# Kernel optimization log

Hardware: AMD Instinct MI355X
Metric: run time of the kernel (lower is better)

The kernel has to match this reference:

```python
import jax, jax.numpy as jnp
import numpy as np

D_MODEL = 2048
D_FF = 8192
N_EXPERTS = 4
B, S = 2, 2048


def setup_inputs() -> dict:
    key = jax.random.key(0)
    ks = jax.random.split(key, 6)
    scale = 0.02
    return {
        "hidden_states": jax.random.normal(ks[0], (B, S, D_MODEL), dtype=jnp.float32),
        "Wr": jax.random.normal(ks[1], (D_MODEL, N_EXPERTS), dtype=jnp.float32) * scale,
        "br": jnp.zeros((N_EXPERTS,), dtype=jnp.float32),
        "Wg": jax.random.normal(ks[2], (N_EXPERTS, D_MODEL, D_FF), dtype=jnp.float32) * scale,
        "Wu": jax.random.normal(ks[3], (N_EXPERTS, D_MODEL, D_FF), dtype=jnp.float32) * scale,
        "Wd": jax.random.normal(ks[4], (N_EXPERTS, D_FF, D_MODEL), dtype=jnp.float32) * scale,
    }


def reference(hidden_states, Wr, br, Wg, Wu, Wd):
    b, s, d = hidden_states.shape
    x = hidden_states.reshape(-1, d)  # [T, d]

    # Router: top-1 over softmax probabilities
    logits = x @ Wr + br                      # [T, E]
    probs = jax.nn.softmax(logits, axis=-1)   # [T, E]
    top_w, top_idx = jax.lax.top_k(probs, 1)  # [T, 1], [T, 1]

    # Mistral gated MLP per expert, computed densely then selected (same math
    # as masked gather -> expert MLP -> masked_scatter with top-1 routing).
    g = jnp.einsum('td,edf->tef', x, Wg)      # [T, E, f]
    u = jnp.einsum('td,edf->tef', x, Wu)      # [T, E, f]
    h = jax.nn.silu(g) * u                    # [T, E, f]
    y = jnp.einsum('tef,efd->ted', h, Wd)     # [T, E, d]

    sel = jnp.take_along_axis(y, top_idx[:, :, None], axis=1)[:, 0]  # [T, d]
    out = sel * top_w                          # scale by top-1 routing weight
    return out.reshape(b, s, d)
```

## Files before the change

kernel.cpp:

```cpp
#include <hip/hip_runtime.h>

#define T_TOK 4096
#define DM 2048
#define DF 8192
#define NE 4
#define BM 256
#define BN 64
#define BKO 32
#define BKN 64
#define MAX_TILES 20
#define PADROWS 256
#define LDK (BKO + 8)
#define NXCD 8

typedef __attribute__((ext_vector_type(8))) short short8;
typedef __attribute__((ext_vector_type(4))) float f32x4;

__device__ __forceinline__ unsigned short f2bf(float f) {
  unsigned int u = __float_as_uint(f);
  u += 0x7fffu + ((u >> 16) & 1u);
  return (unsigned short)(u >> 16);
}

__device__ __forceinline__ void gld_lds16(const unsigned short* g, unsigned short* l) {
  __builtin_amdgcn_global_load_lds(
      (const __attribute__((address_space(1))) unsigned int*)g,
      (__attribute__((address_space(3))) unsigned int*)l, 16, 0, 0);
}

__global__ __launch_bounds__(256) void router_kernel(
    const float* __restrict__ x, const float* __restrict__ Wr,
    const float* __restrict__ br, int* __restrict__ top_idx,
    float* __restrict__ top_w, int* __restrict__ counts) {
  int tok = (blockIdx.x * blockDim.x + threadIdx.x) >> 6;
  int lane = threadIdx.x & 63;
  if (tok >= T_TOK) return;
  const float* xr = x + (size_t)tok * DM;
  float s0 = 0.f, s1 = 0.f, s2 = 0.f, s3 = 0.f;
  for (int j = lane; j < DM; j += 64) {
    float xv = xr[j];
    float4 w = *(const float4*)(Wr + (size_t)j * NE);
    s0 += xv * w.x; s1 += xv * w.y; s2 += xv * w.z; s3 += xv * w.w;
  }
#pragma unroll
  for (int off = 32; off > 0; off >>= 1) {
    s0 += __shfl_xor(s0, off);
    s1 += __shfl_xor(s1, off);
    s2 += __shfl_xor(s2, off);
    s3 += __shfl_xor(s3, off);
  }
  if (lane == 0) {
    float l[NE] = {s0 + br[0], s1 + br[1], s2 + br[2], s3 + br[3]};
    int bi = 0; float bm = l[0];
#pragma unroll
    for (int e = 1; e < NE; e++) if (l[e] > bm) { bm = l[e]; bi = e; }
    float s = 0.f;
#pragma unroll
    for (int e = 0; e < NE; e++) s += __expf(l[e] - bm);
    top_idx[tok] = bi;
    top_w[tok] = 1.0f / s;
    atomicAdd(&counts[bi], 1);
  }
}

__global__ void scan_kernel(const int* __restrict__ counts, int* __restrict__ offs,
                            int* __restrict__ cursors, int* __restrict__ tiles) {
  if (threadIdx.x != 0 || blockIdx.x != 0) return;
  int offv[NE + 1];
  offv[0] = 0;
  for (int e = 0; e < NE; e++) offv[e + 1] = offv[e] + counts[e];
  for (int e = 0; e <= NE; e++) offs[e] = offv[e];
  for (int e = 0; e < NE; e++) cursors[e] = offv[e];
  int nt = 0;
  for (int e = 0; e < NE; e++) {
    int c = counts[e];
    for (int s = 0; s < c; s += BM) {
      tiles[nt * 3 + 0] = e;
      tiles[nt * 3 + 1] = offv[e] + s;
      tiles[nt * 3 + 2] = (c - s < BM) ? (c - s) : BM;
      nt++;
    }
  }
  for (; nt < MAX_TILES; nt++) {
    tiles[nt * 3 + 0] = 0; tiles[nt * 3 + 1] = 0; tiles[nt * 3 + 2] = 0;
  }
}

__global__ __launch_bounds__(256) void scatter_kernel(
    const int* __restrict__ top_idx, int* __restrict__ cursors,
    int* __restrict__ sorted) {
  int t = blockIdx.x * blockDim.x + threadIdx.x;
  if (t >= T_TOK) return;
  int e = top_idx[t];
  int p = atomicAdd(&cursors[e], 1);
  sorted[p] = t;
}

__global__ __launch_bounds__(256) void gather_x_kernel(
    const float* __restrict__ x, const int* __restrict__ sorted,
    unsigned short* __restrict__ xs) {
  const int row = blockIdx.x;
  const int t = threadIdx.x;
  unsigned short* orow = xs + (size_t)row * DM + (t << 3);
  if (row >= T_TOK) {
    short8 z = (short8){0,0,0,0,0,0,0,0};
    *(short8*)orow = z;
    return;
  }
  const float* irow = x + (size_t)sorted[row] * DM + (t << 3);
  float4 a = *(const float4*)irow;
  float4 b = *(const float4*)(irow + 4);
  short8 p;
  p[0] = (short)f2bf(a.x); p[1] = (short)f2bf(a.y);
  p[2] = (short)f2bf(a.z); p[3] = (short)f2bf(a.w);
  p[4] = (short)f2bf(b.x); p[5] = (short)f2bf(b.y);
  p[6] = (short)f2bf(b.z); p[7] = (short)f2bf(b.w);
  *(short8*)orow = p;
}

__global__ __launch_bounds__(256) void transpose_cvt_kernel(
    const float* __restrict__ in, unsigned short* __restrict__ out, int R, int C) {
  __shared__ float tile[64][68];
  const size_t eo = (size_t)blockIdx.z * (size_t)R * (size_t)C;
  const float* inp = in + eo;
  unsigned short* outp = out + eo;
  const int r0 = blockIdx.y << 6, c0 = blockIdx.x << 6;
  const int t = threadIdx.x;
  const int lrow = t >> 4, lcol = (t & 15) << 2;
#pragma unroll
  for (int i = 0; i < 4; i++) {
    float4 v = *(const float4*)(inp + (size_t)(r0 + (i << 4) + lrow) * C + c0 + lcol);
    *(float4*)&tile[(i << 4) + lrow][lcol] = v;
  }
  __syncthreads();
  const int gg = t & 7, cc = t >> 3;
#pragma unroll
  for (int cp = 0; cp < 2; cp++) {
    int c = cc + (cp << 5);
    short8 pv;
#pragma unroll
    for (int i = 0; i < 8; i++) pv[i] = (short)f2bf(tile[(gg << 3) + i][c]);
    *(short8*)(outp + (size_t)(c0 + c) * R + r0 + (gg << 3)) = pv;
  }
}

__global__ __launch_bounds__(512, 4) void gemm1_bf16_kernel(
    const unsigned short* __restrict__ xs, const unsigned short* __restrict__ wg,
    const unsigned short* __restrict__ wu, const int* __restrict__ tiles,
    unsigned short* __restrict__ hbuf) {
  const int bid = blockIdx.x;
  const int xcd = bid & (NXCD - 1);
  const int idx = bid >> 3;
  const int slot = idx % MAX_TILES;
  const int y = (xcd << 4) + idx / MAX_TILES;
  const int n0 = y * BN;

  const int e = tiles[slot * 3 + 0];
  const int row0 = tiles[slot * 3 + 1];
  const int nvalid = tiles[slot * 3 + 2];
  if (nvalid == 0) return;

  __shared__ __align__(16) unsigned short As[BM * BKN];
  __shared__ __align__(16) unsigned short Bg[BN * BKN];
  __shared__ __align__(16) unsigned short Bu[BN * BKN];

  const int t = threadIdx.x;
  const int w = t >> 6, lane = t & 63;
  const int l3 = lane >> 3, l7 = lane & 7;
  const int swz = l7 ^ l3;
  const int lr = lane & 15;
  const int wrow = (w >> 1) << 6, wcol = (w & 1) << 5;

  const unsigned short* wge = wg + (size_t)e * DM * DF;
  const unsigned short* wue = wu + (size_t)e * DM * DF;

  const unsigned short* aSrc = xs + (size_t)(row0 + (w << 5) + l3) * DM + (swz << 3);
  const unsigned short* bgSrc = wge + (size_t)(n0 + (w << 3) + l3) * DM + (swz << 3);
  const unsigned short* buSrc = wue + (size_t)(n0 + (w << 3) + l3) * DM + (swz << 3);

  f32x4 accg[4][2], accu[4][2];
#pragma unroll
  for (int mi = 0; mi < 4; mi++)
#pragma unroll
    for (int ni = 0; ni < 2; ni++) {
      accg[mi][ni] = (f32x4){0.f, 0.f, 0.f, 0.f};
      accu[mi][ni] = (f32x4){0.f, 0.f, 0.f, 0.f};
    }

  for (int k0 = 0; k0 < DM; k0 += BKN) {
#pragma unroll
    for (int j = 0; j < 4; j++)
      gld_lds16(aSrc + (size_t)(j << 3) * DM + k0, &As[(((w << 2) + j) << 9)]);
    gld_lds16(bgSrc + k0, &Bg[w << 9]);
    gld_lds16(buSrc + k0, &Bu[w << 9]);
    __syncthreads();

#pragma unroll
    for (int h = 0; h < 2; h++) {
      const int gbase = (h << 2) + (lane >> 4);
      const int g = gbase ^ (lr & 7);
      short8 af[4], bgf[2], buf2[2];
#pragma unroll
      for (int mi = 0; mi < 4; mi++) {
        int row = wrow + (mi << 4) + lr;
        af[mi] = *(const short8*)&As[(row << 6) + (g << 3)];
      }
#pragma unroll
      for (int ni = 0; ni < 2; ni++) {
        int row = wcol + (ni << 4) + lr;
        bgf[ni]  = *(const short8*)&Bg[(row << 6) + (g << 3)];
        buf2[ni] = *(const short8*)&Bu[(row << 6) + (g << 3)];
      }
#pragma unroll
      for (int mi = 0; mi < 4; mi++)
#pragma unroll
        for (int ni = 0; ni < 2; ni++) {
          accg[mi][ni] = __builtin_amdgcn_mfma_f32_16x16x32_bf16(af[mi], bgf[ni], accg[mi][ni], 0, 0, 0);
          accu[mi][ni] = __builtin_amdgcn_mfma_f32_16x16x32_bf16(af[mi], buf2[ni], accu[mi][ni], 0, 0, 0);
        }
    }
    __syncthreads();
  }

  const int l4 = (lane >> 4) << 2;
#pragma unroll
  for (int mi = 0; mi < 4; mi++) {
#pragma unroll
    for (int r = 0; r < 4; r++) {
      int lrow = wrow + (mi << 4) + l4 + r;
      if (lrow < nvalid) {
        size_t base = (size_t)(row0 + lrow) * DF + n0 + wcol + lr;
#pragma unroll
        for (int ni = 0; ni < 2; ni++) {
          float gv = accg[mi][ni][r];
          float uv = accu[mi][ni][r];
          float hv = (gv / (1.f + __expf(-gv))) * uv;
          hbuf[base + (ni << 4)] = f2bf(hv);
        }
      }
    }
  }
}

__global__ __launch_bounds__(512, 4) void gemm2_bf16_kernel(
    const unsigned short* __restrict__ hbuf, const unsigned short* __restrict__ wd,
    const int* __restrict__ tiles, const int* __restrict__ sorted,
    const float* __restrict__ topw, float* __restrict__ out) {
  const int bid = blockIdx.x;
  const int xcd = bid & (NXCD - 1);
  const int idx = bid >> 3;
  const int slot = idx % MAX_TILES;
  const int y = (xcd << 2) + idx / MAX_TILES;
  const int n0 = y * BN;

  const int e = tiles[slot * 3 + 0];
  const int row0 = tiles[slot * 3 + 1];
  const int nvalid = tiles[slot * 3 + 2];
  if (nvalid == 0) return;

  __shared__ __align__(16) unsigned short As[BM * BKN];
  __shared__ __align__(16) unsigned short Bs[BN * BKN];

  const int t = threadIdx.x;
  const int w = t >> 6, lane = t & 63;
  const int l3 = lane >> 3, l7 = lane & 7;
  const int swz = l7 ^ l3;
  const int lr = lane & 15;
  const int wrow = (w >> 1) << 6, wcol = (w & 1) << 5;

  const unsigned short* wde = wd + (size_t)e * DM * DF;
  const unsigned short* aSrc = hbuf + (size_t)(row0 + (w << 5) + l3) * DF + (swz << 3);
  const unsigned short* bSrc = wde + (size_t)(n0 + (w << 3) + l3) * DF + (swz << 3);

  f32x4 acc[4][2];
#pragma unroll
  for (int mi = 0; mi < 4; mi++)
#pragma unroll
    for (int ni = 0; ni < 2; ni++) acc[mi][ni] = (f32x4){0.f, 0.f, 0.f, 0.f};

  for (int k0 = 0; k0 < DF; k0 += BKN) {
#pragma unroll
    for (int j = 0; j < 4; j++)
      gld_lds16(aSrc + (size_t)(j << 3) * DF + k0, &As[(((w << 2) + j) << 9)]);
    gld_lds16(bSrc + k0, &Bs[w << 9]);
    __syncthreads();

#pragma unroll
    for (int h = 0; h < 2; h++) {
      const int gbase = (h << 2) + (lane >> 4);
      const int g = gbase ^ (lr & 7);
      short8 af[4], bf2[2];
#pragma unroll
      for (int mi = 0; mi < 4; mi++) {
        int row = wrow + (mi << 4) + lr;
        af[mi] = *(const short8*)&As[(row << 6) + (g << 3)];
      }
#pragma unroll
      for (int ni = 0; ni < 2; ni++) {
        int row = wcol + (ni << 4) + lr;
        bf2[ni] = *(const short8*)&Bs[(row << 6) + (g << 3)];
      }
#pragma unroll
      for (int mi = 0; mi < 4; mi++)
#pragma unroll
        for (int ni = 0; ni < 2; ni++)
          acc[mi][ni] = __builtin_amdgcn_mfma_f32_16x16x32_bf16(af[mi], bf2[ni], acc[mi][ni], 0, 0, 0);
    }
    __syncthreads();
  }

  const int l4 = (lane >> 4) << 2;
#pragma unroll
  for (int mi = 0; mi < 4; mi++) {
#pragma unroll
    for (int r = 0; r < 4; r++) {
      int lrow = wrow + (mi << 4) + l4 + r;
      if (lrow < nvalid) {
        int tok = sorted[row0 + lrow];
        float wv = topw[tok];
        size_t base = (size_t)tok * DM + n0 + wcol + lr;
#pragma unroll
        for (int ni = 0; ni < 2; ni++)
          out[base + (ni << 4)] = acc[mi][ni][r] * wv;
      }
    }
  }
}

__global__ __launch_bounds__(512, 4) void gemm1_f32_kernel(
    const float* __restrict__ x, const float* __restrict__ Wg,
    const float* __restrict__ Wu, const int* __restrict__ tiles,
    const int* __restrict__ sorted, unsigned short* __restrict__ hbuf) {
  const int slot = blockIdx.x;
  const int e = tiles[slot * 3 + 0];
  const int row0 = tiles[slot * 3 + 1];
  const int nvalid = tiles[slot * 3 + 2];
  if (nvalid == 0) return;
  const int n0 = blockIdx.y * BN;

  __shared__ __align__(16) unsigned short As[BM][LDK];
  __shared__ __align__(16) unsigned short Bg[BN][LDK];
  __shared__ __align__(16) unsigned short Bu[BN][LDK];

  const int t = threadIdx.x;
  const int arow = t >> 1;
  const int ah = (t & 1) << 4;
  const int atok = (arow < nvalid) ? sorted[row0 + arow] : -1;
  const float* __restrict__ xrow = x + (size_t)(atok >= 0 ? atok : 0) * DM;
  const int bn = t & 63;
  const int bkq = (t >> 6) << 2;

  const size_t eo = (size_t)e * DM * DF;
  const float* __restrict__ Wge = Wg + eo;
  const float* __restrict__ Wue = Wu + eo;

  const int wv = t >> 6, lane = t & 63;
  const int wrow = (wv >> 1) << 6, wcol = (wv & 1) << 5;
  const int lr = lane & 15, lk = (lane >> 4) << 3;

  f32x4 accg[4][2], accu[4][2];
#pragma unroll
  for (int mi = 0; mi < 4; mi++)
#pragma unroll
    for (int ni = 0; ni < 2; ni++) {
      accg[mi][ni] = (f32x4){0.f, 0.f, 0.f, 0.f};
      accu[mi][ni] = (f32x4){0.f, 0.f, 0.f, 0.f};
    }

  for (int k0 = 0; k0 < DM; k0 += BKO) {
#pragma unroll
    for (int j = 0; j < 4; j++) {
      float4 v = make_float4(0.f, 0.f, 0.f, 0.f);
      if (atok >= 0) v = *(const float4*)(xrow + k0 + ah + (j << 2));
      ushort4 pv;
      pv.x = f2bf(v.x); pv.y = f2bf(v.y); pv.z = f2bf(v.z); pv.w = f2bf(v.w);
      *(ushort4*)&As[arow][ah + (j << 2)] = pv;
    }
    {
      const float* pg = Wge + (size_t)(k0 + bkq) * DF + n0 + bn;
      const float* pu = Wue + (size_t)(k0 + bkq) * DF + n0 + bn;
      ushort4 vg, vu;
      vg.x = f2bf(pg[0]);              vu.x = f2bf(pu[0]);
      vg.y = f2bf(pg[(size_t)DF]);     vu.y = f2bf(pu[(size_t)DF]);
      vg.z = f2bf(pg[(size_t)2 * DF]); vu.z = f2bf(pu[(size_t)2 * DF]);
      vg.w = f2bf(pg[(size_t)3 * DF]); vu.w = f2bf(pu[(size_t)3 * DF]);
      *(ushort4*)&Bg[bn][bkq] = vg;
      *(ushort4*)&Bu[bn][bkq] = vu;
    }
    __syncthreads();

    short8 af[4], bgf[2], buf2[2];
#pragma unroll
    for (int mi = 0; mi < 4; mi++)
      af[mi] = *(const short8*)&As[wrow + (mi << 4) + lr][lk];
#pragma unroll
    for (int ni = 0; ni < 2; ni++) {
      bgf[ni]  = *(const short8*)&Bg[wcol + (ni << 4) + lr][lk];
      buf2[ni] = *(const short8*)&Bu[wcol + (ni << 4) + lr][lk];
    }
#pragma unroll
    for (int mi = 0; mi < 4; mi++)
#pragma unroll
      for (int ni = 0; ni < 2; ni++) {
        accg[mi][ni] = __builtin_amdgcn_mfma_f32_16x16x32_bf16(af[mi], bgf[ni], accg[mi][ni], 0, 0, 0);
        accu[mi][ni] = __builtin_amdgcn_mfma_f32_16x16x32_bf16(af[mi], buf2[ni], accu[mi][ni], 0, 0, 0);
      }
    __syncthreads();
  }

  const int l4 = (lane >> 4) << 2;
#pragma unroll
  for (int mi = 0; mi < 4; mi++) {
#pragma unroll
    for (int r = 0; r < 4; r++) {
      int lrow = wrow + (mi << 4) + l4 + r;
      if (lrow < nvalid) {
        size_t base = (size_t)(row0 + lrow) * DF + n0 + wcol + lr;
#pragma unroll
        for (int ni = 0; ni < 2; ni++) {
          float g = accg[mi][ni][r];
          float u = accu[mi][ni][r];
          float hv = (g / (1.f + __expf(-g))) * u;
          hbuf[base + (ni << 4)] = f2bf(hv);
        }
      }
    }
  }
}

__global__ __launch_bounds__(512, 4) void gemm2_f32_kernel(
    const unsigned short* __restrict__ hbuf, const float* __restrict__ Wd,
    const int* __restrict__ tiles, const int* __restrict__ sorted,
    const float* __restrict__ topw, float* __restrict__ out) {
  const int slot = blockIdx.x;
  const int e = tiles[slot * 3 + 0];
  const int row0 = tiles[slot * 3 + 1];
  const int nvalid = tiles[slot * 3 + 2];
  if (nvalid == 0) return;
  const int n0 = blockIdx.y * BN;

  __shared__ __align__(16) unsigned short As[BM][LDK];
  __shared__ __align__(16) unsigned short Bs[BN][LDK];

  const int t = threadIdx.x;
  const int arow = t >> 1;
  const int ah = (t & 1) << 4;
  const int bn = t & 63;
  const int bkq = (t >> 6) << 2;
  const float* __restrict__ Wde = Wd + (size_t)e * DF * DM;

  const int wv = t >> 6, lane = t & 63;
  const int wrow = (wv >> 1) << 6, wcol = (wv & 1) << 5;
  const int lr = lane & 15, lk = (lane >> 4) << 3;

  f32x4 acc[4][2];
#pragma unroll
  for (int mi = 0; mi < 4; mi++)
#pragma unroll
    for (int ni = 0; ni < 2; ni++) acc[mi][ni] = (f32x4){0.f, 0.f, 0.f, 0.f};

  const unsigned short* __restrict__ hrow =
      hbuf + (size_t)(row0 + (arow < nvalid ? arow : 0)) * DF;

  for (int k0 = 0; k0 < DF; k0 += BKO) {
    {
      short8 v0 = (short8){0,0,0,0,0,0,0,0}, v1 = v0;
      if (arow < nvalid) {
        v0 = *(const short8*)(hrow + k0 + ah);
        v1 = *(const short8*)(hrow + k0 + ah + 8);
      }
      *(short8*)&As[arow][ah] = v0;
      *(short8*)&As[arow][ah + 8] = v1;
    }
    {
      const float* pd = Wde + (size_t)(k0 + bkq) * DM + n0 + bn;
      ushort4 vd;
      vd.x = f2bf(pd[0]);
      vd.y = f2bf(pd[(size_t)DM]);
      vd.z = f2bf(pd[(size_t)2 * DM]);
      vd.w = f2bf(pd[(size_t)3 * DM]);
      *(ushort4*)&Bs[bn][bkq] = vd;
    }
    __syncthreads();

    short8 af[4], bf2[2];
#pragma unroll
    for (int mi = 0; mi < 4; mi++)
      af[mi] = *(const short8*)&As[wrow + (mi << 4) + lr][lk];
#pragma unroll
    for (int ni = 0; ni < 2; ni++)
      bf2[ni] = *(const short8*)&Bs[wcol + (ni << 4) + lr][lk];
#pragma unroll
    for (int mi = 0; mi < 4; mi++)
#pragma unroll
      for (int ni = 0; ni < 2; ni++)
        acc[mi][ni] = __builtin_amdgcn_mfma_f32_16x16x32_bf16(af[mi], bf2[ni], acc[mi][ni], 0, 0, 0);
    __syncthreads();
  }

  const int l4 = (lane >> 4) << 2;
#pragma unroll
  for (int mi = 0; mi < 4; mi++) {
#pragma unroll
    for (int r = 0; r < 4; r++) {
      int lrow = wrow + (mi << 4) + l4 + r;
      if (lrow < nvalid) {
        int tok = sorted[row0 + lrow];
        float w = topw[tok];
        size_t base = (size_t)tok * DM + n0 + wcol + lr;
#pragma unroll
        for (int ni = 0; ni < 2; ni++)
          out[base + (ni << 4)] = acc[mi][ni][r] * w;
      }
    }
  }
}

extern "C" void kernel_launch(void* const* d_in, const int* in_sizes, int n_in,
                              void* d_out, int out_size, void* d_ws, size_t ws_size,
                              hipStream_t stream) {
  const float* x  = (const float*)d_in[0];
  const float* Wr = (const float*)d_in[1];
  const float* br = (const float*)d_in[2];
  const float* Wg = (const float*)d_in[3];
  const float* Wu = (const float*)d_in[4];
  const float* Wd = (const float*)d_in[5];
  float* out = (float*)d_out;

  const size_t XS_ELEMS = (size_t)(T_TOK + PADROWS) * DM;
  const size_t HB_ELEMS = (size_t)(T_TOK + PADROWS) * DF;
  const size_t W_ELEMS  = (size_t)NE * DM * DF;
  const size_t NEED = (XS_ELEMS + HB_ELEMS + 3 * W_ELEMS) * 2 + (1 << 20);

  if (ws_size >= NEED) {
    unsigned short* xs = (unsigned short*)d_ws;
    unsigned short* hb = xs + XS_ELEMS;
    unsigned short* wg = hb + HB_ELEMS;
    unsigned short* wu = wg + W_ELEMS;
    unsigned short* wd = wu + W_ELEMS;
    int* meta = (int*)(wd + W_ELEMS);
    int* top_idx = meta;
    int* sorted  = meta + 4096;
    int* counts  = meta + 8192;
    int* offs    = meta + 8196;
    int* cursors = meta + 8201;
    int* tiles   = meta + 8208;
    float* topw  = (float*)(meta + 8320);

    hipMemsetAsync(counts, 0, NE * sizeof(int), stream);
    router_kernel<<<dim3((T_TOK * 64) / 256), 256, 0, stream>>>(x, Wr, br, top_idx, topw, counts);
    scan_kernel<<<1, 1, 0, stream>>>(counts, offs, cursors, tiles);
    scatter_kernel<<<dim3(T_TOK / 256), 256, 0, stream>>>(top_idx, cursors, sorted);
    gather_x_kernel<<<dim3(T_TOK + PADROWS), 256, 0, stream>>>(x, sorted, xs);
    transpose_cvt_kernel<<<dim3(DF / 64, DM / 64, NE), 256, 0, stream>>>(Wg, wg, DM, DF);
    transpose_cvt_kernel<<<dim3(DF / 64, DM / 64, NE), 256, 0, stream>>>(Wu, wu, DM, DF);
    transpose_cvt_kernel<<<dim3(DM / 64, DF / 64, NE), 256, 0, stream>>>(Wd, wd, DF, DM);
    gemm1_bf16_kernel<<<dim3(MAX_TILES * (DF / BN)), 512, 0, stream>>>(xs, wg, wu, tiles, hb);
    gemm2_bf16_kernel<<<dim3(MAX_TILES * (DM / BN)), 512, 0, stream>>>(hb, wd, tiles, sorted, topw, out);
  } else {
    const size_t H_BYTES = (size_t)T_TOK * DF * 2;
    unsigned short* hbuf = (unsigned short*)d_ws;
    int* meta = (int*)((char*)d_ws + H_BYTES);
    int* top_idx = meta;
    int* sorted  = meta + 4096;
    int* counts  = meta + 8192;
    int* offs    = meta + 8196;
    int* cursors = meta + 8201;
    int* tiles   = meta + 8208;
    float* topw  = (float*)(meta + 8320);

    hipMemsetAsync(counts, 0, NE * sizeof(int), stream);
    router_kernel<<<dim3((T_TOK * 64) / 256), 256, 0, stream>>>(x, Wr, br, top_idx, topw, counts);
    scan_kernel<<<1, 1, 0, stream>>>(counts, offs, cursors, tiles);
    scatter_kernel<<<dim3(T_TOK / 256), 256, 0, stream>>>(top_idx, cursors, sorted);
    gemm1_f32_kernel<<<dim3(MAX_TILES, DF / BN), 512, 0, stream>>>(x, Wg, Wu, tiles, sorted, hbuf);
    gemm2_f32_kernel<<<dim3(MAX_TILES, DM / BN), 512, 0, stream>>>(hbuf, Wd, tiles, sorted, topw, out);
  }
}
```

Measured before the change: 1.081 ms.

## Double-buffer bf16 expert GEMMs with 256x128 tiles and warp-specialized loads

Both bf16 grouped GEMMs move from a 256x64 tile with one LDS buffer to a 256x128 tile with two LDS buffers. The next K-slice is prefetched via global_load_lds while MFMAs run on the current one, and the per-iteration barriers drop from two to one. Loads are now split by warp role (A, gate and up weights are each fetched by dedicated warps), and the XCD-aware block remapping is replaced by a plain 2D grid. This doubles accumulator registers and LDS per block and lowers the occupancy target to 2, and losing the XCD swizzle may reduce L2 reuse of weights.

```diff
diff --git a/kernel.cpp b/kernel.cpp
--- a/kernel.cpp
+++ b/kernel.cpp
@@ -6,12 +6,12 @@
 #define NE 4
 #define BM 256
 #define BN 64
+#define GBN 128
+#define GBK 64
 #define BKO 32
-#define BKN 64
 #define MAX_TILES 20
 #define PADROWS 256
 #define LDK (BKO + 8)
-#define NXCD 8
 
 typedef __attribute__((ext_vector_type(8))) short short8;
 typedef __attribute__((ext_vector_type(4))) float f32x4;
@@ -144,92 +144,114 @@
   }
 }
 
-__global__ __launch_bounds__(512, 4) void gemm1_bf16_kernel(
+__global__ __launch_bounds__(512, 2) void gemm1_bf16_kernel(
     const unsigned short* __restrict__ xs, const unsigned short* __restrict__ wg,
     const unsigned short* __restrict__ wu, const int* __restrict__ tiles,
     unsigned short* __restrict__ hbuf) {
-  const int bid = blockIdx.x;
-  const int xcd = bid & (NXCD - 1);
-  const int idx = bid >> 3;
-  const int slot = idx % MAX_TILES;
-  const int y = (xcd << 4) + idx / MAX_TILES;
-  const int n0 = y * BN;
-
+  const int slot = blockIdx.x;
   const int e = tiles[slot * 3 + 0];
   const int row0 = tiles[slot * 3 + 1];
   const int nvalid = tiles[slot * 3 + 2];
   if (nvalid == 0) return;
-
-  __shared__ __align__(16) unsigned short As[BM * BKN];
-  __shared__ __align__(16) unsigned short Bg[BN * BKN];
-  __shared__ __align__(16) unsigned short Bu[BN * BKN];
+  const int n0 = blockIdx.y * GBN;
+
+  __shared__ __align__(16) unsigned short As[2][BM * GBK];
+  __shared__ __align__(16) unsigned short Bg[2][GBN * GBK];
+  __shared__ __align__(16) unsigned short Bu[2][GBN * GBK];
 
   const int t = threadIdx.x;
   const int w = t >> 6, lane = t & 63;
-  const int l3 = lane >> 3, l7 = lane & 7;
-  const int swz = l7 ^ l3;
+  const int l3 = lane >> 3;
+  const int swz = (lane & 7) ^ l3;
   const int lr = lane & 15;
-  const int wrow = (w >> 1) << 6, wcol = (w & 1) << 5;
+  const int wm = w >> 2, wn = w & 3;
 
   const unsigned short* wge = wg + (size_t)e * DM * DF;
   const unsigned short* wue = wu + (size_t)e * DM * DF;
 
-  const unsigned short* aSrc = xs + (size_t)(row0 + (w << 5) + l3) * DM + (swz << 3);
-  const unsigned short* bgSrc = wge + (size_t)(n0 + (w << 3) + l3) * DM + (swz << 3);
-  const unsigned short* buSrc = wue + (size_t)(n0 + (w << 3) + l3) * DM + (swz << 3);
-
-  f32x4 accg[4][2], accu[4][2];
-#pragma unroll
-  for (int mi = 0; mi < 4; mi++)
+  const unsigned short* sA = xs + (size_t)(row0 + (w << 6) + l3) * DM + (swz << 3);
+  const unsigned short* sBg = wge + (size_t)(n0 + ((w - 4) << 6) + l3) * DM + (swz << 3);
+  const unsigned short* sBu = wue + (size_t)(n0 + ((w - 6) << 6) + l3) * DM + (swz << 3);
+
+  f32x4 accg[8][2], accu[8][2];
+#pragma unroll
+  for (int mi = 0; mi < 8; mi++)
 #pragma unroll
     for (int ni = 0; ni < 2; ni++) {
       accg[mi][ni] = (f32x4){0.f, 0.f, 0.f, 0.f};
       accu[mi][ni] = (f32x4){0.f, 0.f, 0.f, 0.f};
     }
 
-  for (int k0 = 0; k0 < DM; k0 += BKN) {
-#pragma unroll
-    for (int j = 0; j < 4; j++)
-      gld_lds16(aSrc + (size_t)(j << 3) * DM + k0, &As[(((w << 2) + j) << 9)]);
-    gld_lds16(bgSrc + k0, &Bg[w << 9]);
-    gld_lds16(buSrc + k0, &Bu[w << 9]);
+#define G1_STAGE(B, K0)                                                        \
+  do {                                                                         \
+    if (w < 4) {                                                               \
+      unsigned short* d = &As[B][(w << 6) << 6];                               \
+      _Pragma("unroll")                                                        \
+      for (int j = 0; j < 8; j++)                                              \
+        gld_lds16(sA + (size_t)(j << 3) * DM + (K0), d + (j << 9));            \
+    } else if (w < 6) {                                                        \
+      unsigned short* d = &Bg[B][((w - 4) << 6) << 6];                         \
+      _Pragma("unroll")                                                        \
+      for (int j = 0; j < 8; j++)                                              \
+        gld_lds16(sBg + (size_t)(j << 3) * DM + (K0), d + (j << 9));           \
+    } else {                                                                   \
+      unsigned short* d = &Bu[B][((w - 6) << 6) << 6];                         \
+      _Pragma("unroll")                                                        \
+      for (int j = 0; j < 8; j++)                                              \
+        gld_lds16(sBu + (size_t)(j << 3) * DM + (K0), d + (j << 9));           \
+    }                                                                          \
+  } while (0)
+
+#define G1_COMPUTE(B)                                                          \
+  do {                                                                         \
+    _Pragma("unroll")                                                          \
+    for (int h = 0; h < 2; h++) {                                              \
+      const int gq = (h << 2) + (lane >> 4);                                   \
+      const int g = gq ^ (lr & 7);                                             \
+      short8 af[8], bgf[2], buf2[2];                                           \
+      _Pragma("unroll")                                                        \
+      for (int mi = 0; mi < 8; mi++) {                                         \
+        int row = (wm << 7) + (mi << 4) + lr;                                  \
+        af[mi] = *(const short8*)&As[B][(row << 6) + (g << 3)];                \
+      }                                                                        \
+      _Pragma("unroll")                                                        \
+      for (int ni = 0; ni < 2; ni++) {                                         \
+        int row = (wn << 5) + (ni << 4) + lr;                                  \
+        bgf[ni]  = *(const short8*)&Bg[B][(row << 6) + (g << 3)];              \
+        buf2[ni] = *(const short8*)&Bu[B][(row << 6) + (g << 3)];              \
+      }                                                                        \
+      _Pragma("unroll")                                                        \
+      for (int mi = 0; mi < 8; mi++)                                           \
+        _Pragma("unroll")                                                      \
+        for (int ni = 0; ni < 2; ni++) {                                       \
+          accg[mi][ni] = __builtin_amdgcn_mfma_f32_16x16x32_bf16(              \
+              af[mi], bgf[ni], accg[mi][ni], 0, 0, 0);                         \
+          accu[mi][ni] = __builtin_amdgcn_mfma_f32_16x16x32_bf16(              \
+              af[mi], buf2[ni], accu[mi][ni], 0, 0, 0);                        \
+        }                                                                      \
+    }                                                                          \
+  } while (0)
+
+  const int NK = DM / GBK;
+  int cur = 0;
+  G1_STAGE(0, 0);
+  __syncthreads();
+  for (int kt = 0; kt < NK - 1; ++kt) {
+    G1_STAGE(cur ^ 1, (kt + 1) * GBK);
+    G1_COMPUTE(cur);
     __syncthreads();
-
-#pragma unroll
-    for (int h = 0; h < 2; h++) {
-      const int gbase = (h << 2) + (lane >> 4);
-      const int g = gbase ^ (lr & 7);
-      short8 af[4], bgf[2], buf2[2];
-#pragma unroll
-      for (int mi = 0; mi < 4; mi++) {
-        int row = wrow + (mi << 4) + lr;
-        af[mi] = *(const short8*)&As[(row << 6) + (g << 3)];
-      }
-#pragma unroll
-      for (int ni = 0; ni < 2; ni++) {
-        int row = wcol + (ni << 4) + lr;
-        bgf[ni]  = *(const short8*)&Bg[(row << 6) + (g << 3)];
-        buf2[ni] = *(const short8*)&Bu[(row << 6) + (g << 3)];
-      }
-#pragma unroll
-      for (int mi = 0; mi < 4; mi++)
-#pragma unroll
-        for (int ni = 0; ni < 2; ni++) {
-          accg[mi][ni] = __builtin_amdgcn_mfma_f32_16x16x32_bf16(af[mi], bgf[ni], accg[mi][ni], 0, 0, 0);
-          accu[mi][ni] = __builtin_amdgcn_mfma_f32_16x16x32_bf16(af[mi], buf2[ni], accu[mi][ni], 0, 0, 0);
-        }
-    }
-    __syncthreads();
-  }
+    cur ^= 1;
+  }
+  G1_COMPUTE(cur);
 
   const int l4 = (lane >> 4) << 2;
 #pragma unroll
-  for (int mi = 0; mi < 4; mi++) {
+  for (int mi = 0; mi < 8; mi++) {
 #pragma unroll
     for (int r = 0; r < 4; r++) {
-      int lrow = wrow + (mi << 4) + l4 + r;
+      int lrow = (wm << 7) + (mi << 4) + l4 + r;
       if (lrow < nvalid) {
-        size_t base = (size_t)(row0 + lrow) * DF + n0 + wcol + lr;
+        size_t base = (size_t)(row0 + lrow) * DF + n0 + (wn << 5) + lr;
 #pragma unroll
         for (int ni = 0; ni < 2; ni++) {
           float gv = accg[mi][ni][r];
@@ -240,91 +262,112 @@
       }
     }
   }
-}
-
-__global__ __launch_bounds__(512, 4) void gemm2_bf16_kernel(
+#undef G1_STAGE
+#undef G1_COMPUTE
+}
+
+__global__ __launch_bounds__(512, 2) void gemm2_bf16_kernel(
     const unsigned short* __restrict__ hbuf, const unsigned short* __restrict__ wd,
     const int* __restrict__ tiles, const int* __restrict__ sorted,
     const float* __restrict__ topw, float* __restrict__ out) {
-  const int bid = blockIdx.x;
-  const int xcd = bid & (NXCD - 1);
-  const int idx = bid >> 3;
-  const int slot = idx % MAX_TILES;
-  const int y = (xcd << 2) + idx / MAX_TILES;
-  const int n0 = y * BN;
-
+  const int slot = blockIdx.x;
   const int e = tiles[slot * 3 + 0];
   const int row0 = tiles[slot * 3 + 1];
   const int nvalid = tiles[slot * 3 + 2];
   if (nvalid == 0) return;
-
-  __shared__ __align__(16) unsigned short As[BM * BKN];
-  __shared__ __align__(16) unsigned short Bs[BN * BKN];
+  const int n0 = blockIdx.y * GBN;
+
+  __shared__ __align__(16) unsigned short As[2][BM * GBK];
+  __shared__ __align__(16) unsigned short Bs[2][GBN * GBK];
 
   const int t = threadIdx.x;
   const int w = t >> 6, lane = t & 63;
-  const int l3 = lane >> 3, l7 = lane & 7;
-  const int swz = l7 ^ l3;
+  const int l3 = lane >> 3;
+  const int swz = (lane & 7) ^ l3;
   const int lr = lane & 15;
-  const int wrow = (w >> 1) << 6, wcol = (w & 1) << 5;
+  const int wm = w >> 2, wn = w & 3;
 
   const unsigned short* wde = wd + (size_t)e * DM * DF;
-  const unsigned short* aSrc = hbuf + (size_t)(row0 + (w << 5) + l3) * DF + (swz << 3);
-  const unsigned short* bSrc = wde + (size_t)(n0 + (w << 3) + l3) * DF + (swz << 3);
-
-  f32x4 acc[4][2];
-#pragma unroll
-  for (int mi = 0; mi < 4; mi++)
+  const unsigned short* sA = hbuf + (size_t)(row0 + (w << 6) + l3) * DF + (swz << 3);
+  const unsigned short* sB = wde + (size_t)(n0 + ((w - 4) << 5) + l3) * DF + (swz << 3);
+
+  f32x4 acc[8][2];
+#pragma unroll
+  for (int mi = 0; mi < 8; mi++)
 #pragma unroll
     for (int ni = 0; ni < 2; ni++) acc[mi][ni] = (f32x4){0.f, 0.f, 0.f, 0.f};
 
-  for (int k0 = 0; k0 < DF; k0 += BKN) {
-#pragma unroll
-    for (int j = 0; j < 4; j++)
-      gld_lds16(aSrc + (size_t)(j << 3) * DF + k0, &As[(((w << 2) + j) << 9)]);
-    gld_lds16(bSrc + k0, &Bs[w << 9]);
+#define G2_STAGE(B, K0)                                                        \
+  do {                                                                         \
+    if (w < 4) {                                                               \
+      unsigned short* d = &As[B][(w << 6) << 6];                               \
+      _Pragma("unroll")                                                        \
+      for (int j = 0; j < 8; j++)                                              \
+        gld_lds16(sA + (size_t)(j << 3) * DF + (K0), d + (j << 9));            \
+    } else {                                                                   \
+      unsigned short* d = &Bs[B][((w - 4) << 5) << 6];                         \
+      _Pragma("unroll")                                                        \
+      for (int j = 0; j < 4; j++)                                              \
+        gld_lds16(sB + (size_t)(j << 3) * DF + (K0), d + (j << 9));            \
+    }                                                                          \
+  } while (0)
+
+#define G2_COMPUTE(B)                                                          \
+  do {                                                                         \
+    _Pragma("unroll")                                                          \
+    for (int h = 0; h < 2; h++) {                                              \
+      const int gq = (h << 2) + (lane >> 4);                                   \
+      const int g = gq ^ (lr & 7);                                             \
+      short8 af[8], bf2[2];                                                    \
+      _Pragma("unroll")                                                        \
+      for (int mi = 0; mi < 8; mi++) {                                         \
+        int row = (wm << 7) + (mi << 4) + lr;                                  \
+        af[mi] = *(const short8*)&As[B][(row << 6) + (g << 3)];                \
+      }                                                                        \
+      _Pragma("unroll")                                                        \
+      for (int ni = 0; ni < 2; ni++) {                                         \
+        int row = (wn << 5) + (ni << 4) + lr;                                  \
+        bf2[ni] = *(const short8*)&Bs[B][(row << 6) + (g << 3)];               \
+      }                                                                        \
+      _Pragma("unroll")                                                        \
+      for (int mi = 0; mi < 8; mi++)                                           \
+        _Pragma("unroll")                                                      \
+        for (int ni = 0; ni < 2; ni++)                                         \
+          acc[mi][ni] = __builtin_amdgcn_mfma_f32_16x16x32_bf16(               \
+              af[mi], bf2[ni], acc[mi][ni], 0, 0, 0);                          \
+    }                                                                          \
+  } while (0)
+
+  const int NK = DF / GBK;
+  int cur = 0;
+  G2_STAGE(0, 0);
+  __syncthreads();
+  for (int kt = 0; kt < NK - 1; ++kt) {
+    G2_STAGE(cur ^ 1, (kt + 1) * GBK);
+    G2_COMPUTE(cur);
     __syncthreads();
-
-#pragma unroll
-    for (int h = 0; h < 2; h++) {
-      const int gbase = (h << 2) + (lane >> 4);
-      const int g = gbase ^ (lr & 7);
-      short8 af[4], bf2[2];
-#pragma unroll
-      for (int mi = 0; mi < 4; mi++) {
-        int row = wrow + (mi << 4) + lr;
-        af[mi] = *(const short8*)&As[(row << 6) + (g << 3)];
-      }
-#pragma unroll
-      for (int ni = 0; ni < 2; ni++) {
-        int row = wcol + (ni << 4) + lr;
-        bf2[ni] = *(const short8*)&Bs[(row << 6) + (g << 3)];
-      }
-#pragma unroll
-      for (int mi = 0; mi < 4; mi++)
-#pragma unroll
-        for (int ni = 0; ni < 2; ni++)
-          acc[mi][ni] = __builtin_amdgcn_mfma_f32_16x16x32_bf16(af[mi], bf2[ni], acc[mi][ni], 0, 0, 0);
-    }
-    __syncthreads();
-  }
+    cur ^= 1;
+  }
+  G2_COMPUTE(cur);
 
   const int l4 = (lane >> 4) << 2;
 #pragma unroll
-  for (int mi = 0; mi < 4; mi++) {
+  for (int mi = 0; mi < 8; mi++) {
 #pragma unroll
     for (int r = 0; r < 4; r++) {
-      int lrow = wrow + (mi << 4) + l4 + r;
+      int lrow = (wm << 7) + (mi << 4) + l4 + r;
       if (lrow < nvalid) {
         int tok = sorted[row0 + lrow];
         float wv = topw[tok];
-        size_t base = (size_t)tok * DM + n0 + wcol + lr;
+        size_t base = (size_t)tok * DM + n0 + (wn << 5) + lr;
 #pragma unroll
         for (int ni = 0; ni < 2; ni++)
           out[base + (ni << 4)] = acc[mi][ni][r] * wv;
       }
     }
   }
+#undef G2_STAGE
+#undef G2_COMPUTE
 }
 
 __global__ __launch_bounds__(512, 4) void gemm1_f32_kernel(
@@ -555,8 +598,8 @@
     transpose_cvt_kernel<<<dim3(DF / 64, DM / 64, NE), 256, 0, stream>>>(Wg, wg, DM, DF);
     transpose_cvt_kernel<<<dim3(DF / 64, DM / 64, NE), 256, 0, stream>>>(Wu, wu, DM, DF);
     transpose_cvt_kernel<<<dim3(DM / 64, DF / 64, NE), 256, 0, stream>>>(Wd, wd, DF, DM);
-    gemm1_bf16_kernel<<<dim3(MAX_TILES * (DF / BN)), 512, 0, stream>>>(xs, wg, wu, tiles, hb);
-    gemm2_bf16_kernel<<<dim3(MAX_TILES * (DM / BN)), 512, 0, stream>>>(hb, wd, tiles, sorted, topw, out);
+    gemm1_bf16_kernel<<<dim3(MAX_TILES, DF / GBN), 512, 0, stream>>>(xs, wg, wu, tiles, hb);
+    gemm2_bf16_kernel<<<dim3(MAX_TILES, DM / GBN), 512, 0, stream>>>(hb, wd, tiles, sorted, topw, out);
   } else {
     const size_t H_BYTES = (size_t)T_TOK * DF * 2;
     unsigned short* hbuf = (unsigned short*)d_ws;
```

Result: faster. 1.048 ms (-3.1%).
